# Kernel optimization log

Hardware: AMD Instinct MI355X
Metric: run time of the kernel (lower is better)

Reference implementation:

```python
import jax, jax.numpy as jnp
from jax import lax
import numpy as np

B, C, T, D = 262144, 3, 10, 5
H = 8  # per-direction hidden size


def setup_inputs() -> dict:
    key = jax.random.key(0)
    ks = jax.random.split(key, 7)
    s = 1.0 / np.sqrt(H)  # pytorch default uniform(-1/sqrt(H),1/sqrt(H)); use scaled normal
    return {
        "x": jax.random.normal(ks[0], (B, C, T, D), jnp.float32),
        "Wih0": jax.random.normal(ks[1], (2, 4 * H, C * D), jnp.float32) * s,
        "Wih_rest": jax.random.normal(ks[2], (2, 2, 4 * H, 2 * H), jnp.float32) * s,
        "Whh": jax.random.normal(ks[3], (3, 2, 4 * H, H), jnp.float32) * s,
        "b": jax.random.normal(ks[4], (3, 2, 4 * H), jnp.float32) * s,  # b_ih + b_hh combined
        "Wout": jax.random.normal(ks[5], (1, 2 * H * T), jnp.float32) * 0.05,
        "bout": jnp.zeros((1,), jnp.float32),
    }


def _lstm_dir(h_in, Wih, Whh_d, b_d, reverse):
    # h_in: [B,T,Din]; precompute input projections for all timesteps at once
    xg = jnp.einsum('btd,gd->btg', h_in, Wih) + b_d  # [B,T,4H]

    def step(carry, xt):
        h, c = carry
        g = xt + h @ Whh_d.T  # [B,4H]
        i, f, gg, o = jnp.split(g, 4, axis=-1)  # pytorch gate order i,f,g,o
        i = jax.nn.sigmoid(i)
        f = jax.nn.sigmoid(f)
        gg = jnp.tanh(gg)
        o = jax.nn.sigmoid(o)
        c = f * c + i * gg
        h = o * jnp.tanh(c)
        return (h, c), h

    nb = h_in.shape[0]
    h0 = jnp.zeros((nb, H), h_in.dtype)
    _, ys = lax.scan(step, (h0, h0), jnp.swapaxes(xg, 0, 1), reverse=reverse)
    return jnp.swapaxes(ys, 0, 1)  # [B,T,H]


def reference(x, Wih0, Wih_rest, Whh, b, Wout, bout):
    # x: [B,C,T,D] -> [B,T,C*D]
    h = jnp.transpose(x, (0, 2, 1, 3)).reshape(x.shape[0], T, C * D)
    for l in range(3):
        Wf = Wih0[0] if l == 0 else Wih_rest[l - 1, 0]
        Wb = Wih0[1] if l == 0 else Wih_rest[l - 1, 1]
        fwd = _lstm_dir(h, Wf, Whh[l, 0], b[l, 0], False)
        bwd = _lstm_dir(h, Wb, Whh[l, 1], b[l, 1], True)
        h = jnp.concatenate([fwd, bwd], axis=-1)  # [B,T,2H]
    flat = h.reshape(h.shape[0], T * 2 * H)  # [B,160]
    out = flat @ Wout.T + bout  # [B,1]
    return out.squeeze()
```

## Files before the change

### kernel.cpp

```cpp
#include <hip/hip_runtime.h>

#define TPB 256
#define L2E 1.44269504f

typedef float f32x4 __attribute__((ext_vector_type(4)));
typedef short s16x8 __attribute__((ext_vector_type(8)));

#define SWZ(v, m) __int_as_float(__builtin_amdgcn_ds_swizzle(__float_as_int(v), ((m) << 10) | 31))

__device__ __forceinline__ unsigned pack_split(float v) {
    unsigned b  = __float_as_uint(v);
    unsigned hi = b >> 16;
    float    hf = __uint_as_float(b & 0xFFFF0000u);
    unsigned lob = __float_as_uint(v - hf) & 0xFFFF0000u;
    return lob | hi;
}

__global__ void prep_kernel(const float* __restrict__ Wih0,
                            const float* __restrict__ Wih_rest,
                            const float* __restrict__ Whh,
                            const float* __restrict__ bW,
                            unsigned* __restrict__ wsBF,
                            float* __restrict__ wsWH,
                            float* __restrict__ wsBIAS)
{
    const int tid = threadIdx.x;
    for (int seg = 0; seg < 6; ++seg) {
        const int l = seg >> 1, dir = seg & 1;
        {
            const int lane_ = tid & 63, part = (tid >> 6) & 1, nt = tid >> 7;
            const int u = nt * 16 + (lane_ & 15);
            const float sc = ((u >> 3) == 2) ? (-2.0f * L2E) : (-L2E);
            #pragma unroll
            for (int ip = 0; ip < 4; ++ip) {
                const int d = (lane_ >> 4) * 4 + ip;
                float w;
                if (l == 0) w = (d < 15) ? Wih0[dir * 480 + u * 15 + d] : 0.0f;
                else        w = Wih_rest[((l - 1) * 2 + dir) * 512 + u * 16 + d];
                w *= sc;
                unsigned b = __float_as_uint(w);
                unsigned v16;
                if (part == 0) v16 = b >> 16;
                else {
                    float hf = __uint_as_float(b & 0xFFFF0000u);
                    v16 = __float_as_uint(w - hf) >> 16;
                }
                wsBF[seg * 4096 + ((nt * 2 + part) * 64 + lane_) * 4 + ip] = v16 | (v16 << 16);
            }
        }
        {
            const int jj = tid >> 5, rr = tid & 31, g = rr >> 3, m = rr & 7;
            const float sc = (g == 2) ? (-2.0f * L2E) : (-L2E);
            wsWH[seg * 256 + jj * 32 + rr] = sc * Whh[seg * 256 + (g * 8 + jj) * 8 + (jj ^ m)];
        }
        if (tid < 32) {
            const float sc = ((tid >> 3) == 2) ? (-2.0f * L2E) : (-L2E);
            wsBIAS[seg * 32 + tid] = sc * bW[seg * 32 + tid];
        }
    }
}

template<int DIR, bool LAST>
__device__ __forceinline__ void run_seg(const unsigned* __restrict__ XSin,
                                        unsigned* __restrict__ XSout,
                                        const unsigned* __restrict__ bfSeg,
                                        const float* __restrict__ whSeg,
                                        const float* __restrict__ biasSeg,
                                        const float* __restrict__ Wout,
                                        float* __restrict__ G2,
                                        float& accOut, int lane, int wid)
{
    const int r   = lane & 15;
    const int kb  = lane >> 4;
    const int grp = lane >> 3;
    const int j   = lane & 7;
    const int elg = wid * 8 + grp;

    s16x8 Bf00 = *(const s16x8*)&bfSeg[(0 * 64 + lane) * 4];
    s16x8 Bf01 = *(const s16x8*)&bfSeg[(1 * 64 + lane) * 4];
    s16x8 Bf10 = *(const s16x8*)&bfSeg[(2 * 64 + lane) * 4];
    s16x8 Bf11 = *(const s16x8*)&bfSeg[(3 * 64 + lane) * 4];
    const float bs0 = biasSeg[r];
    const float bs1 = biasSeg[16 + r];

    const int AI0 = ((r >> 3) * 32 + wid * 8 + (r & 7)) * 17 + kb * 4;
    const int SBW = wid * 576 + (kb >> 1) * 288 + (kb & 1) * 4 * 36 + r;
    const int GBW = wid * 576 + grp * 36 + j;

    float gx[4][10];
    #pragma unroll
    for (int m = 0; m < 5; ++m) {
        s16x8 A = *(const s16x8*)&XSin[AI0 + m * 1088];
        f32x4 acc0 = {bs0, bs0, bs0, bs0};
        f32x4 acc1 = {bs1, bs1, bs1, bs1};
        acc0 = __builtin_amdgcn_mfma_f32_16x16x32_bf16(A, Bf00, acc0, 0, 0, 0);
        acc0 = __builtin_amdgcn_mfma_f32_16x16x32_bf16(A, Bf01, acc0, 0, 0, 0);
        acc1 = __builtin_amdgcn_mfma_f32_16x16x32_bf16(A, Bf10, acc1, 0, 0, 0);
        acc1 = __builtin_amdgcn_mfma_f32_16x16x32_bf16(A, Bf11, acc1, 0, 0, 0);
        #pragma unroll
        for (int q = 0; q < 4; ++q) {
            G2[SBW + q * 36]      = acc0[q];
            G2[SBW + q * 36 + 16] = acc1[q];
        }
        #pragma unroll
        for (int t2 = 0; t2 < 2; ++t2)
            #pragma unroll
            for (int g = 0; g < 4; ++g)
                gx[g][2 * m + t2] = G2[GBW + t2 * 288 + g * 8];
    }

    float wh[32];
    #pragma unroll
    for (int q = 0; q < 8; ++q)
        *(f32x4*)&wh[q * 4] = *(const f32x4*)&whSeg[j * 32 + q * 4];

    float cst = 0.0f, hn = 0.0f;
    #pragma unroll
    for (int tt = 0; tt < 10; ++tt) {
        const int s = DIR ? (9 - tt) : tt;
        float g0 = gx[0][s], g1 = gx[1][s], g2v = gx[2][s], g3 = gx[3][s];
        if (tt > 0) {
            const float h1 = SWZ(hn, 1), h2 = SWZ(hn, 2), h3 = SWZ(hn, 3),
                        h4 = SWZ(hn, 4), h5 = SWZ(hn, 5), h6 = SWZ(hn, 6), h7 = SWZ(hn, 7);
            g0 = fmaf(wh[0], hn, g0);  g0 = fmaf(wh[1], h1, g0);
            g0 = fmaf(wh[2], h2, g0);  g0 = fmaf(wh[3], h3, g0);
            g0 = fmaf(wh[4], h4, g0);  g0 = fmaf(wh[5], h5, g0);
            g0 = fmaf(wh[6], h6, g0);  g0 = fmaf(wh[7], h7, g0);
            g1 = fmaf(wh[8], hn, g1);  g1 = fmaf(wh[9], h1, g1);
            g1 = fmaf(wh[10], h2, g1); g1 = fmaf(wh[11], h3, g1);
            g1 = fmaf(wh[12], h4, g1); g1 = fmaf(wh[13], h5, g1);
            g1 = fmaf(wh[14], h6, g1); g1 = fmaf(wh[15], h7, g1);
            g2v = fmaf(wh[16], hn, g2v); g2v = fmaf(wh[17], h1, g2v);
            g2v = fmaf(wh[18], h2, g2v); g2v = fmaf(wh[19], h3, g2v);
            g2v = fmaf(wh[20], h4, g2v); g2v = fmaf(wh[21], h5, g2v);
            g2v = fmaf(wh[22], h6, g2v); g2v = fmaf(wh[23], h7, g2v);
            g3 = fmaf(wh[24], hn, g3);  g3 = fmaf(wh[25], h1, g3);
            g3 = fmaf(wh[26], h2, g3);  g3 = fmaf(wh[27], h3, g3);
            g3 = fmaf(wh[28], h4, g3);  g3 = fmaf(wh[29], h5, g3);
            g3 = fmaf(wh[30], h6, g3);  g3 = fmaf(wh[31], h7, g3);
        }
        const float ig = __builtin_amdgcn_rcpf(1.0f + __builtin_amdgcn_exp2f(g0));
        const float fg = __builtin_amdgcn_rcpf(1.0f + __builtin_amdgcn_exp2f(g1));
        const float gg = 2.0f * __builtin_amdgcn_rcpf(1.0f + __builtin_amdgcn_exp2f(g2v)) - 1.0f;
        const float og = __builtin_amdgcn_rcpf(1.0f + __builtin_amdgcn_exp2f(g3));
        cst = fg * cst + ig * gg;
        const float ec = __builtin_amdgcn_exp2f(-2.0f * L2E * cst);
        const float th = 2.0f * __builtin_amdgcn_rcpf(1.0f + ec) - 1.0f;
        hn = og * th;

        if (LAST) accOut += hn * Wout[s * 16 + DIR * 8 + j];
        else      XSout[(s * 32 + elg) * 17 + DIR * 8 + j] = pack_split(hn);
    }
}

__global__ __launch_bounds__(TPB, 3)
void lstm_kernel(const float* __restrict__ x,
                 const unsigned* __restrict__ wsBF,
                 const float* __restrict__ wsWH,
                 const float* __restrict__ wsBIAS,
                 const float* __restrict__ Wout,
                 const float* __restrict__ bout,
                 float* __restrict__ out)
{
    __shared__ __align__(16) unsigned XA[5440];
    __shared__ __align__(16) unsigned XB[5440];
    __shared__ __align__(16) float    G2[2304];

    const int tid  = threadIdx.x;
    const int lane = tid & 63, wid = tid >> 6;

    const float* xw = x + (size_t)blockIdx.x * 4800 + wid * 1200;
    for (int i = lane; i < 1200; i += 64) {
        int e = wid * 8 + i / 150, rr = i % 150;
        int c = rr / 50, r2 = rr % 50, t = r2 / 5, d = r2 % 5;
        XA[(t * 32 + e) * 17 + c * 5 + d] = pack_split(xw[i]);
    }
    for (int i = lane; i < 80; i += 64) {
        int t = i >> 3, e = wid * 8 + (i & 7);
        XA[(t * 32 + e) * 17 + 15] = 0u;
    }

    float accOut = 0.0f;
    run_seg<0, false>(XA, XB, wsBF + 0 * 4096, wsWH + 0 * 256, wsBIAS + 0 * 32, Wout, G2, accOut, lane, wid);
    run_seg<1, false>(XA, XB, wsBF + 1 * 4096, wsWH + 1 * 256, wsBIAS + 1 * 32, Wout, G2, accOut, lane, wid);
    run_seg<0, false>(XB, XA, wsBF + 2 * 4096, wsWH + 2 * 256, wsBIAS + 2 * 32, Wout, G2, accOut, lane, wid);
    run_seg<1, false>(XB, XA, wsBF + 3 * 4096, wsWH + 3 * 256, wsBIAS + 3 * 32, Wout, G2, accOut, lane, wid);
    run_seg<0, true >(XA, XB, wsBF + 4 * 4096, wsWH + 4 * 256, wsBIAS + 4 * 32, Wout, G2, accOut, lane, wid);
    run_seg<1, true >(XA, XB, wsBF + 5 * 4096, wsWH + 5 * 256, wsBIAS + 5 * 32, Wout, G2, accOut, lane, wid);

    accOut += __shfl_xor(accOut, 1);
    accOut += __shfl_xor(accOut, 2);
    accOut += __shfl_xor(accOut, 4);
    if ((lane & 7) == 0)
        out[(size_t)blockIdx.x * 32 + wid * 8 + (lane >> 3)] = accOut + bout[0];
}

extern "C" void kernel_launch(void* const* d_in, const int* in_sizes, int n_in,
                              void* d_out, int out_size, void* d_ws, size_t ws_size,
                              hipStream_t stream) {
    const float* x        = (const float*)d_in[0];
    const float* Wih0     = (const float*)d_in[1];
    const float* Wih_rest = (const float*)d_in[2];
    const float* Whh      = (const float*)d_in[3];
    const float* b        = (const float*)d_in[4];
    const float* Wout     = (const float*)d_in[5];
    const float* bout     = (const float*)d_in[6];
    float* out = (float*)d_out;

    unsigned* wsBF   = (unsigned*)d_ws;
    float*    wsWH   = (float*)d_ws + 6 * 4096;
    float*    wsBIAS = (float*)d_ws + 6 * 4096 + 6 * 256;

    prep_kernel<<<1, TPB, 0, stream>>>(Wih0, Wih_rest, Whh, b, wsBF, wsWH, wsBIAS);

    const int nblocks = out_size / 32;
    lstm_kernel<<<nblocks, TPB, 0, stream>>>(x, wsBF, wsWH, wsBIAS, Wout, bout, out);
}
```

Measured before the change: 295.1 us.

## Fuse forward and backward LSTM directions per layer with in-place LDS buffer

Each layer now runs the forward and backward recurrences interleaved in one loop, which doubles independent work per step to hide latency in the serial recurrence. The input projections for both directions are computed from the same A fragment before the loop, so the two directions share it. The double LDS buffer becomes a single XOR-swizzled 16-wide buffer that is written in place, and the gate scratch is made per-wave with vector stores. Cross-lane hidden-state exchange moves mostly from ds_swizzle to DPP, Wout is preloaded into registers, and launch bounds go from 3 to 5 blocks. The trade-off is more register pressure from twice the live gate state under a tighter occupancy target, which risks spills. In-place overwrite of the input buffer relies on all reads of a layer finishing first within each wave.

Measured after the change: 833.0 us. 2.82x slower.

```diff
diff --git a/kernel.cpp b/kernel.cpp
--- a/kernel.cpp
+++ b/kernel.cpp
@@ -7,6 +7,16 @@
 typedef short s16x8 __attribute__((ext_vector_type(8)));
 
 #define SWZ(v, m) __int_as_float(__builtin_amdgcn_ds_swizzle(__float_as_int(v), ((m) << 10) | 31))
+
+#define DPP_X1 0xB1
+#define DPP_X2 0x4E
+#define DPP_X3 0x1B
+#define DPP_X7 0x141
+template<int CTRL>
+__device__ __forceinline__ float DPPX(float v) {
+    int i = __float_as_int(v);
+    return __int_as_float(__builtin_amdgcn_update_dpp(i, i, CTRL, 0xF, 0xF, false));
+}
 
 __device__ __forceinline__ unsigned pack_split(float v) {
     unsigned b  = __float_as_uint(v);
@@ -15,6 +25,8 @@
     unsigned lob = __float_as_uint(v - hf) & 0xFFFF0000u;
     return lob | hi;
 }
+
+#define XIDX(t, e, col) ((((t) * 32 + (e)) << 4) | ((col) ^ (((e) & 3) << 2)))
 
 __global__ void prep_kernel(const float* __restrict__ Wih0,
                             const float* __restrict__ Wih_rest,
@@ -60,15 +72,17 @@
     }
 }
 
-template<int DIR, bool LAST>
-__device__ __forceinline__ void run_seg(const unsigned* __restrict__ XSin,
-                                        unsigned* __restrict__ XSout,
-                                        const unsigned* __restrict__ bfSeg,
-                                        const float* __restrict__ whSeg,
-                                        const float* __restrict__ biasSeg,
-                                        const float* __restrict__ Wout,
-                                        float* __restrict__ G2,
-                                        float& accOut, int lane, int wid)
+template<bool LAST>
+__device__ __forceinline__ void run_layer(unsigned* __restrict__ XS,
+                                          const unsigned* __restrict__ bfF,
+                                          const unsigned* __restrict__ bfB,
+                                          const float* __restrict__ whFg,
+                                          const float* __restrict__ whBg,
+                                          const float* __restrict__ biasF,
+                                          const float* __restrict__ biasB,
+                                          const float* __restrict__ Wout,
+                                          float* __restrict__ g2w,
+                                          float& accOut, int lane, int wid)
 {
     const int r   = lane & 15;
     const int kb  = lane >> 4;
@@ -76,84 +90,132 @@
     const int j   = lane & 7;
     const int elg = wid * 8 + grp;
 
-    s16x8 Bf00 = *(const s16x8*)&bfSeg[(0 * 64 + lane) * 4];
-    s16x8 Bf01 = *(const s16x8*)&bfSeg[(1 * 64 + lane) * 4];
-    s16x8 Bf10 = *(const s16x8*)&bfSeg[(2 * 64 + lane) * 4];
-    s16x8 Bf11 = *(const s16x8*)&bfSeg[(3 * 64 + lane) * 4];
-    const float bs0 = biasSeg[r];
-    const float bs1 = biasSeg[16 + r];
-
-    const int AI0 = ((r >> 3) * 32 + wid * 8 + (r & 7)) * 17 + kb * 4;
-    const int SBW = wid * 576 + (kb >> 1) * 288 + (kb & 1) * 4 * 36 + r;
-    const int GBW = wid * 576 + grp * 36 + j;
-
-    float gx[4][10];
+    const int AI0 = (((r >> 3) * 32 + wid * 8 + (r & 7)) << 4) + ((kb ^ (r & 3)) << 2);
+    const int sb0 = (kb >> 1) * 256 + r * 8 + (kb & 1) * 4;
+    const int gb  = j * 8 + grp;
+
+    float gxF[4][10], gxB[4][10];
+    {
+        s16x8 BF0 = *(const s16x8*)&bfF[(0 * 64 + lane) * 4];
+        s16x8 BF1 = *(const s16x8*)&bfF[(1 * 64 + lane) * 4];
+        s16x8 BF2 = *(const s16x8*)&bfF[(2 * 64 + lane) * 4];
+        s16x8 BF3 = *(const s16x8*)&bfF[(3 * 64 + lane) * 4];
+        s16x8 BB0 = *(const s16x8*)&bfB[(0 * 64 + lane) * 4];
+        s16x8 BB1 = *(const s16x8*)&bfB[(1 * 64 + lane) * 4];
+        s16x8 BB2 = *(const s16x8*)&bfB[(2 * 64 + lane) * 4];
+        s16x8 BB3 = *(const s16x8*)&bfB[(3 * 64 + lane) * 4];
+        const float bf0 = biasF[r], bf1 = biasF[16 + r];
+        const float bb0 = biasB[r], bb1 = biasB[16 + r];
+
+        #pragma unroll
+        for (int m = 0; m < 5; ++m) {
+            s16x8 A = *(const s16x8*)&XS[AI0 + m * 1024];
+
+            f32x4 a0 = {bf0, bf0, bf0, bf0}, a1 = {bf1, bf1, bf1, bf1};
+            a0 = __builtin_amdgcn_mfma_f32_16x16x32_bf16(A, BF0, a0, 0, 0, 0);
+            a0 = __builtin_amdgcn_mfma_f32_16x16x32_bf16(A, BF1, a0, 0, 0, 0);
+            a1 = __builtin_amdgcn_mfma_f32_16x16x32_bf16(A, BF2, a1, 0, 0, 0);
+            a1 = __builtin_amdgcn_mfma_f32_16x16x32_bf16(A, BF3, a1, 0, 0, 0);
+            *(f32x4*)&g2w[sb0]       = a0;
+            *(f32x4*)&g2w[sb0 + 128] = a1;
+            #pragma unroll
+            for (int t2 = 0; t2 < 2; ++t2)
+                #pragma unroll
+                for (int g = 0; g < 4; ++g)
+                    gxF[g][2 * m + t2] = g2w[t2 * 256 + g * 64 + gb];
+
+            f32x4 c0 = {bb0, bb0, bb0, bb0}, c1 = {bb1, bb1, bb1, bb1};
+            c0 = __builtin_amdgcn_mfma_f32_16x16x32_bf16(A, BB0, c0, 0, 0, 0);
+            c0 = __builtin_amdgcn_mfma_f32_16x16x32_bf16(A, BB1, c0, 0, 0, 0);
+            c1 = __builtin_amdgcn_mfma_f32_16x16x32_bf16(A, BB2, c1, 0, 0, 0);
+            c1 = __builtin_amdgcn_mfma_f32_16x16x32_bf16(A, BB3, c1, 0, 0, 0);
+            *(f32x4*)&g2w[sb0]       = c0;
+            *(f32x4*)&g2w[sb0 + 128] = c1;
+            #pragma unroll
+            for (int t2 = 0; t2 < 2; ++t2)
+                #pragma unroll
+                for (int g = 0; g < 4; ++g)
+                    gxB[g][2 * m + t2] = g2w[t2 * 256 + g * 64 + gb];
+        }
+    }
+
+    float whF[32], whB[32];
     #pragma unroll
-    for (int m = 0; m < 5; ++m) {
-        s16x8 A = *(const s16x8*)&XSin[AI0 + m * 1088];
-        f32x4 acc0 = {bs0, bs0, bs0, bs0};
-        f32x4 acc1 = {bs1, bs1, bs1, bs1};
-        acc0 = __builtin_amdgcn_mfma_f32_16x16x32_bf16(A, Bf00, acc0, 0, 0, 0);
-        acc0 = __builtin_amdgcn_mfma_f32_16x16x32_bf16(A, Bf01, acc0, 0, 0, 0);
-        acc1 = __builtin_amdgcn_mfma_f32_16x16x32_bf16(A, Bf10, acc1, 0, 0, 0);
-        acc1 = __builtin_amdgcn_mfma_f32_16x16x32_bf16(A, Bf11, acc1, 0, 0, 0);
+    for (int q = 0; q < 8; ++q) {
+        *(f32x4*)&whF[q * 4] = *(const f32x4*)&whFg[j * 32 + q * 4];
+        *(f32x4*)&whB[q * 4] = *(const f32x4*)&whBg[j * 32 + q * 4];
+    }
+
+    float woutF[10], woutB[10];
+    if (LAST) {
         #pragma unroll
-        for (int q = 0; q < 4; ++q) {
-            G2[SBW + q * 36]      = acc0[q];
-            G2[SBW + q * 36 + 16] = acc1[q];
-        }
-        #pragma unroll
-        for (int t2 = 0; t2 < 2; ++t2)
-            #pragma unroll
-            for (int g = 0; g < 4; ++g)
-                gx[g][2 * m + t2] = G2[GBW + t2 * 288 + g * 8];
-    }
-
-    float wh[32];
-    #pragma unroll
-    for (int q = 0; q < 8; ++q)
-        *(f32x4*)&wh[q * 4] = *(const f32x4*)&whSeg[j * 32 + q * 4];
-
-    float cst = 0.0f, hn = 0.0f;
+        for (int t = 0; t < 10; ++t) {
+            woutF[t] = Wout[t * 16 + j];
+            woutB[t] = Wout[t * 16 + 8 + j];
+        }
+    }
+
+    float hF = 0.0f, cF = 0.0f, hB = 0.0f, cB = 0.0f;
     #pragma unroll
     for (int tt = 0; tt < 10; ++tt) {
-        const int s = DIR ? (9 - tt) : tt;
-        float g0 = gx[0][s], g1 = gx[1][s], g2v = gx[2][s], g3 = gx[3][s];
+        const int sF = tt, sB = 9 - tt;
+        float aF0 = gxF[0][sF], aF1 = gxF[1][sF], aF2 = gxF[2][sF], aF3 = gxF[3][sF];
+        float aB0 = gxB[0][sB], aB1 = gxB[1][sB], aB2 = gxB[2][sB], aB3 = gxB[3][sB];
         if (tt > 0) {
-            const float h1 = SWZ(hn, 1), h2 = SWZ(hn, 2), h3 = SWZ(hn, 3),
-                        h4 = SWZ(hn, 4), h5 = SWZ(hn, 5), h6 = SWZ(hn, 6), h7 = SWZ(hn, 7);
-            g0 = fmaf(wh[0], hn, g0);  g0 = fmaf(wh[1], h1, g0);
-            g0 = fmaf(wh[2], h2, g0);  g0 = fmaf(wh[3], h3, g0);
-            g0 = fmaf(wh[4], h4, g0);  g0 = fmaf(wh[5], h5, g0);
-            g0 = fmaf(wh[6], h6, g0);  g0 = fmaf(wh[7], h7, g0);
-            g1 = fmaf(wh[8], hn, g1);  g1 = fmaf(wh[9], h1, g1);
-            g1 = fmaf(wh[10], h2, g1); g1 = fmaf(wh[11], h3, g1);
-            g1 = fmaf(wh[12], h4, g1); g1 = fmaf(wh[13], h5, g1);
-            g1 = fmaf(wh[14], h6, g1); g1 = fmaf(wh[15], h7, g1);
-            g2v = fmaf(wh[16], hn, g2v); g2v = fmaf(wh[17], h1, g2v);
-            g2v = fmaf(wh[18], h2, g2v); g2v = fmaf(wh[19], h3, g2v);
-            g2v = fmaf(wh[20], h4, g2v); g2v = fmaf(wh[21], h5, g2v);
-            g2v = fmaf(wh[22], h6, g2v); g2v = fmaf(wh[23], h7, g2v);
-            g3 = fmaf(wh[24], hn, g3);  g3 = fmaf(wh[25], h1, g3);
-            g3 = fmaf(wh[26], h2, g3);  g3 = fmaf(wh[27], h3, g3);
-            g3 = fmaf(wh[28], h4, g3);  g3 = fmaf(wh[29], h5, g3);
-            g3 = fmaf(wh[30], h6, g3);  g3 = fmaf(wh[31], h7, g3);
-        }
-        const float ig = __builtin_amdgcn_rcpf(1.0f + __builtin_amdgcn_exp2f(g0));
-        const float fg = __builtin_amdgcn_rcpf(1.0f + __builtin_amdgcn_exp2f(g1));
-        const float gg = 2.0f * __builtin_amdgcn_rcpf(1.0f + __builtin_amdgcn_exp2f(g2v)) - 1.0f;
-        const float og = __builtin_amdgcn_rcpf(1.0f + __builtin_amdgcn_exp2f(g3));
-        cst = fg * cst + ig * gg;
-        const float ec = __builtin_amdgcn_exp2f(-2.0f * L2E * cst);
-        const float th = 2.0f * __builtin_amdgcn_rcpf(1.0f + ec) - 1.0f;
-        hn = og * th;
-
-        if (LAST) accOut += hn * Wout[s * 16 + DIR * 8 + j];
-        else      XSout[(s * 32 + elg) * 17 + DIR * 8 + j] = pack_split(hn);
-    }
-}
-
-__global__ __launch_bounds__(TPB, 3)
+            float hsF[8], hsB[8];
+            hsF[0] = hF;
+            hsF[1] = DPPX<DPP_X1>(hF);
+            hsF[2] = DPPX<DPP_X2>(hF);
+            hsF[3] = DPPX<DPP_X3>(hF);
+            hsF[4] = SWZ(hF, 4);
+            hsF[5] = DPPX<DPP_X1>(hsF[4]);
+            hsF[6] = DPPX<DPP_X2>(hsF[4]);
+            hsF[7] = DPPX<DPP_X7>(hF);
+            hsB[0] = hB;
+            hsB[1] = DPPX<DPP_X1>(hB);
+            hsB[2] = DPPX<DPP_X2>(hB);
+            hsB[3] = DPPX<DPP_X3>(hB);
+            hsB[4] = SWZ(hB, 4);
+            hsB[5] = DPPX<DPP_X1>(hsB[4]);
+            hsB[6] = DPPX<DPP_X2>(hsB[4]);
+            hsB[7] = DPPX<DPP_X7>(hB);
+            #pragma unroll
+            for (int m = 0; m < 8; ++m) {
+                aF0 = fmaf(whF[m],      hsF[m], aF0);
+                aB0 = fmaf(whB[m],      hsB[m], aB0);
+                aF1 = fmaf(whF[8 + m],  hsF[m], aF1);
+                aB1 = fmaf(whB[8 + m],  hsB[m], aB1);
+                aF2 = fmaf(whF[16 + m], hsF[m], aF2);
+                aB2 = fmaf(whB[16 + m], hsB[m], aB2);
+                aF3 = fmaf(whF[24 + m], hsF[m], aF3);
+                aB3 = fmaf(whB[24 + m], hsB[m], aB3);
+            }
+        }
+        const float igF = __builtin_amdgcn_rcpf(1.0f + __builtin_amdgcn_exp2f(aF0));
+        const float fgF = __builtin_amdgcn_rcpf(1.0f + __builtin_amdgcn_exp2f(aF1));
+        const float ggF = 2.0f * __builtin_amdgcn_rcpf(1.0f + __builtin_amdgcn_exp2f(aF2)) - 1.0f;
+        const float ogF = __builtin_amdgcn_rcpf(1.0f + __builtin_amdgcn_exp2f(aF3));
+        const float igB = __builtin_amdgcn_rcpf(1.0f + __builtin_amdgcn_exp2f(aB0));
+        const float fgB = __builtin_amdgcn_rcpf(1.0f + __builtin_amdgcn_exp2f(aB1));
+        const float ggB = 2.0f * __builtin_amdgcn_rcpf(1.0f + __builtin_amdgcn_exp2f(aB2)) - 1.0f;
+        const float ogB = __builtin_amdgcn_rcpf(1.0f + __builtin_amdgcn_exp2f(aB3));
+        cF = fmaf(fgF, cF, igF * ggF);
+        cB = fmaf(fgB, cB, igB * ggB);
+        const float ecF = __builtin_amdgcn_exp2f(-2.0f * L2E * cF);
+        const float ecB = __builtin_amdgcn_exp2f(-2.0f * L2E * cB);
+        hF = ogF * (2.0f * __builtin_amdgcn_rcpf(1.0f + ecF) - 1.0f);
+        hB = ogB * (2.0f * __builtin_amdgcn_rcpf(1.0f + ecB) - 1.0f);
+
+        if (LAST) {
+            accOut += hF * woutF[sF] + hB * woutB[sB];
+        } else {
+            XS[XIDX(sF, elg, j)]     = pack_split(hF);
+            XS[XIDX(sB, elg, 8 + j)] = pack_split(hB);
+        }
+    }
+}
+
+__global__ __launch_bounds__(TPB, 5)
 void lstm_kernel(const float* __restrict__ x,
                  const unsigned* __restrict__ wsBF,
                  const float* __restrict__ wsWH,
@@ -162,9 +224,8 @@
                  const float* __restrict__ bout,
                  float* __restrict__ out)
 {
-    __shared__ __align__(16) unsigned XA[5440];
-    __shared__ __align__(16) unsigned XB[5440];
-    __shared__ __align__(16) float    G2[2304];
+    __shared__ __align__(16) unsigned XA[5120];
+    __shared__ __align__(16) float    G2[2048];
 
     const int tid  = threadIdx.x;
     const int lane = tid & 63, wid = tid >> 6;
@@ -173,20 +234,21 @@
     for (int i = lane; i < 1200; i += 64) {
         int e = wid * 8 + i / 150, rr = i % 150;
         int c = rr / 50, r2 = rr % 50, t = r2 / 5, d = r2 % 5;
-        XA[(t * 32 + e) * 17 + c * 5 + d] = pack_split(xw[i]);
+        XA[XIDX(t, e, c * 5 + d)] = pack_split(xw[i]);
     }
     for (int i = lane; i < 80; i += 64) {
         int t = i >> 3, e = wid * 8 + (i & 7);
-        XA[(t * 32 + e) * 17 + 15] = 0u;
-    }
-
+        XA[XIDX(t, e, 15)] = 0u;
+    }
+
+    float* g2w = &G2[wid * 512];
     float accOut = 0.0f;
-    run_seg<0, false>(XA, XB, wsBF + 0 * 4096, wsWH + 0 * 256, wsBIAS + 0 * 32, Wout, G2, accOut, lane, wid);
-    run_seg<1, false>(XA, XB, wsBF + 1 * 4096, wsWH + 1 * 256, wsBIAS + 1 * 32, Wout, G2, accOut, lane, wid);
-    run_seg<0, false>(XB, XA, wsBF + 2 * 4096, wsWH + 2 * 256, wsBIAS + 2 * 32, Wout, G2, accOut, lane, wid);
-    run_seg<1, false>(XB, XA, wsBF + 3 * 4096, wsWH + 3 * 256, wsBIAS + 3 * 32, Wout, G2, accOut, lane, wid);
-    run_seg<0, true >(XA, XB, wsBF + 4 * 4096, wsWH + 4 * 256, wsBIAS + 4 * 32, Wout, G2, accOut, lane, wid);
-    run_seg<1, true >(XA, XB, wsBF + 5 * 4096, wsWH + 5 * 256, wsBIAS + 5 * 32, Wout, G2, accOut, lane, wid);
+    run_layer<false>(XA, wsBF + 0 * 4096, wsBF + 1 * 4096, wsWH + 0 * 256, wsWH + 1 * 256,
+                     wsBIAS + 0 * 32, wsBIAS + 1 * 32, Wout, g2w, accOut, lane, wid);
+    run_layer<false>(XA, wsBF + 2 * 4096, wsBF + 3 * 4096, wsWH + 2 * 256, wsWH + 3 * 256,
+                     wsBIAS + 2 * 32, wsBIAS + 3 * 32, Wout, g2w, accOut, lane, wid);
+    run_layer<true >(XA, wsBF + 4 * 4096, wsBF + 5 * 4096, wsWH + 4 * 256, wsWH + 5 * 256,
+                     wsBIAS + 4 * 32, wsBIAS + 5 * 32, Wout, g2w, accOut, lane, wid);
 
     accOut += __shfl_xor(accOut, 1);
     accOut += __shfl_xor(accOut, 2);
```
